# Optimization experiments

Hardware: AMD Instinct MI355X
Metric: run time of the kernel (lower is better)

## Reference

```python
import jax, jax.numpy as jnp
import numpy as np

EPS = 1e-6  # GLOBAL_EPS
D_QK = 192
ATTN_DIM = 768


def setup_inputs() -> dict:
    key = jax.random.key(0)
    ks = jax.random.split(key, 12)
    B, C, H, W = 16, 192, 56, 56
    d_qk, d_v = D_QK, 2 * D_QK
    attn_dim, inner = ATTN_DIM, d_v
    r = lambda k, s, sc=0.05: jax.random.normal(k, s, dtype=jnp.float32) * sc
    return {
        "x": jax.random.normal(ks[0], (B, C, H, W), dtype=jnp.float32),
        "proj_w": r(ks[1], (attn_dim, C)),          # 1x1 conv + BN folded
        "proj_b": r(ks[2], (attn_dim,)),
        "dwc_w": r(ks[3], (attn_dim, 1, 3, 3)),     # depthwise 3x3, BN folded
        "dwc_b": r(ks[4], (attn_dim,)),
        "g_w": r(ks[5], (inner, attn_dim)),          # ConvGate pointwise conv1d
        "g_b": r(ks[6], (inner,)),
        "an_w": 1.0 + r(ks[7], (inner,)),            # RMSNorm weight
        "sv": 1.0 + r(ks[8], (inner,)),              # Scale(inner, (1, inner, 1))
        "out_w": r(ks[9], (C, inner)),               # 1x1 conv + BN folded
        "out_b": r(ks[10], (C,)),
    }


def reference(x, proj_w, proj_b, dwc_w, dwc_b, g_w, g_b, an_w, sv, out_w, out_b):
    B, C, H, W = x.shape
    d_qk = D_QK
    # proj: ConvNorm 1x1 (conv + BN folded to affine)
    y = jnp.einsum("bchw,oc->bohw", x, proj_w) + proj_b[None, :, None, None]
    # dwc: RepConv depthwise 3x3 with residual (res=True)
    dw = jax.lax.conv_general_dilated(
        y, dwc_w, window_strides=(1, 1), padding="SAME",
        dimension_numbers=("NCHW", "OIHW", "NCHW"),
        feature_group_count=ATTN_DIM)
    y = dw + dwc_b[None, :, None, None] + y
    # flatten spatial -> tokens, split q/k/v along channels
    xs = y.reshape(B, ATTN_DIM, H * W)            # (B, attn_dim, N)
    q, k, v = xs[:, :d_qk], xs[:, d_qk:2 * d_qk], xs[:, 2 * d_qk:]
    # linear_attn: feature map = silu, scale = N**-0.5
    qf = jax.nn.silu(q)                            # (B, d_qk, N)
    kf = jax.nn.silu(k)
    N = H * W
    s = N ** -0.5
    # use_linear branch (N >> d): z = kT.mean(-2,True) @ q + eps ; attn = (v s)(kT s) q
    z = jnp.einsum("bd,bdn->bn", kf.mean(-1), qf)[:, None, :] + EPS  # (B, 1, N)
    vk = jnp.einsum("bvn,bdn->bvd", v * s, kf * s)  # (B, d_v, d_qk)
    attn = jnp.einsum("bvd,bdn->bvn", vk, qf) / z   # (B, d_v, N)
    # gate: pointwise conv1d on full projected features + sigmoid
    gate = jax.nn.sigmoid(jnp.einsum("bcn,oc->bon", xs, g_w) + g_b[None, :, None])
    attn = attn * gate
    # attn_norm (RMS over channels) + scale_v(v) residual
    rms = jnp.sqrt(jnp.mean(attn * attn, axis=1, keepdims=True) + EPS)
    attn = attn / rms * an_w[None, :, None] + v * sv[None, :, None]
    # out: ConvNorm 1x1 back to dim
    o = attn.reshape(B, -1, H, W)
    return jnp.einsum("bchw,oc->bohw", o, out_w) + out_b[None, :, None, None]
```

## Files before the change

kernel.cpp:

```cpp
#include <hip/hip_runtime.h>
#include <hip/hip_bf16.h>

typedef unsigned short u16;
typedef __attribute__((ext_vector_type(8))) short bf16x8;
typedef __attribute__((ext_vector_type(4))) float f32x4;

constexpr int B_ = 16, C_ = 192, H_ = 56, W_ = 56;
constexpr int N_ = H_ * W_;
constexpr int NP = 3200;
constexpr int A_ = 768;
constexpr int Dq = 192;
constexpr int Vd = 384;
constexpr float EPSf = 1e-6f;

union U8 { bf16x8 v; u16 s[8]; unsigned u[4]; };

__device__ __forceinline__ float bits2f(u16 u) {
  return __uint_as_float(((unsigned)u) << 16);
}
__device__ __forceinline__ u16 f2bits(float f) {
  __hip_bfloat16 h = __float2bfloat16(f);
  u16 u;
  __builtin_memcpy(&u, &h, sizeof(u));
  return u;
}
__device__ __forceinline__ float silu_f(float v) { return v / (1.0f + __expf(-v)); }
__device__ __forceinline__ float sigm_f(float v) { return 1.0f / (1.0f + __expf(-v)); }

__device__ __forceinline__ f32x4 MFMA(bf16x8 a, bf16x8 b, f32x4 c) {
  return __builtin_amdgcn_mfma_f32_16x16x32_bf16(a, b, c, 0, 0, 0);
}
__device__ __forceinline__ int swz(int row) { return (row & 7) ^ ((row >> 3) & 7); }

__global__ __launch_bounds__(256) void k_prep(const float* __restrict__ pw,
                                              const float* __restrict__ gw,
                                              const float* __restrict__ ow,
                                              u16* __restrict__ pwb,
                                              u16* __restrict__ gwb,
                                              u16* __restrict__ owb) {
  const int bid = blockIdx.x;
  const size_t base = ((size_t)bid * 256 + threadIdx.x) * 8;
  const float* src;
  u16* dst;
  size_t off;
  if (bid < 72) { src = pw; dst = pwb; off = base; }
  else if (bid < 216) { src = gw; dst = gwb; off = base - 147456; }
  else { src = ow; dst = owb; off = base - 442368; }
  float4 v0 = *(const float4*)&src[off];
  float4 v1 = *(const float4*)&src[off + 4];
  U8 r;
  r.s[0] = f2bits(v0.x); r.s[1] = f2bits(v0.y); r.s[2] = f2bits(v0.z); r.s[3] = f2bits(v0.w);
  r.s[4] = f2bits(v1.x); r.s[5] = f2bits(v1.y); r.s[6] = f2bits(v1.z); r.s[7] = f2bits(v1.w);
  *(bf16x8*)&dst[off] = r.v;
}

__global__ __launch_bounds__(256) void k_proj(const float* __restrict__ x,
                                              const u16* __restrict__ pwb,
                                              const float* __restrict__ pb,
                                              u16* __restrict__ y0t) {
  const int n0 = blockIdx.x * 64;
  const int oy = blockIdx.y;
  const int b = blockIdx.z;
  __shared__ u16 Xt[64][200];
  __shared__ u16 Wa[256][32];
  const int t = threadIdx.x;
  const int lane = t & 63, wid = t >> 6;
  const int fr = lane & 15, fg = lane >> 4;

  {
    const int p = t & 31, co = t >> 5;
    const float* xb = x + (size_t)b * C_ * N_ + n0 + 2 * p;
#pragma unroll
    for (int rnd = 0; rnd < 3; ++rnd) {
      const int c0 = rnd * 64 + co * 8;
      float2 v[8];
#pragma unroll
      for (int i = 0; i < 8; ++i) v[i] = *(const float2*)&xb[(size_t)(c0 + i) * N_];
      U8 r0, r1;
#pragma unroll
      for (int i = 0; i < 8; ++i) { r0.s[i] = f2bits(v[i].x); r1.s[i] = f2bits(v[i].y); }
      *(bf16x8*)&Xt[2 * p][c0] = r0.v;
      *(bf16x8*)&Xt[2 * p + 1][c0] = r1.v;
    }
  }

  f32x4 acc[4][4];
#pragma unroll
  for (int mi = 0; mi < 4; ++mi)
#pragma unroll
    for (int ni = 0; ni < 4; ++ni) acc[mi][ni] = (f32x4){0.f, 0.f, 0.f, 0.f};

  const int orow_c = t >> 2, oct_c = t & 3;
  U8 wreg[4];
#pragma unroll
  for (int jj = 0; jj < 4; ++jj)
    wreg[jj].v = *(const bf16x8*)&pwb[(size_t)(oy * 256 + orow_c + 64 * jj) * C_ + oct_c * 8];

  for (int ks = 0; ks < 6; ++ks) {
    __syncthreads();
#pragma unroll
    for (int jj = 0; jj < 4; ++jj) {
      const int orow = orow_c + 64 * jj;
      const int sw = (orow >> 1) & 3;
      *(bf16x8*)&Wa[orow][(oct_c ^ sw) * 8] = wreg[jj].v;
    }
    __syncthreads();
    if (ks < 5) {
#pragma unroll
      for (int jj = 0; jj < 4; ++jj)
        wreg[jj].v = *(const bf16x8*)&pwb[(size_t)(oy * 256 + orow_c + 64 * jj) * C_ +
                                          (ks + 1) * 32 + oct_c * 8];
    }
    bf16x8 bfrag[4];
#pragma unroll
    for (int ni = 0; ni < 4; ++ni)
      bfrag[ni] = *(const bf16x8*)&Xt[ni * 16 + fr][ks * 32 + fg * 8];
    __builtin_amdgcn_s_setprio(1);
#pragma unroll
    for (int mi = 0; mi < 4; ++mi) {
      const int ar = wid * 64 + mi * 16 + fr;
      bf16x8 a = *(const bf16x8*)&Wa[ar][(fg ^ ((ar >> 1) & 3)) * 8];
#pragma unroll
      for (int ni = 0; ni < 4; ++ni) acc[mi][ni] = MFMA(a, bfrag[ni], acc[mi][ni]);
    }
    __builtin_amdgcn_s_setprio(0);
  }
#pragma unroll
  for (int mi = 0; mi < 4; ++mi) {
    const int o4 = oy * 256 + wid * 64 + mi * 16 + fg * 4;
    const float b0 = pb[o4], b1 = pb[o4 + 1], b2 = pb[o4 + 2], b3 = pb[o4 + 3];
#pragma unroll
    for (int ni = 0; ni < 4; ++ni) {
      const int n = n0 + ni * 16 + fr;
      ushort4 pk;
      pk.x = f2bits(acc[mi][ni][0] + b0);
      pk.y = f2bits(acc[mi][ni][1] + b1);
      pk.z = f2bits(acc[mi][ni][2] + b2);
      pk.w = f2bits(acc[mi][ni][3] + b3);
      *(ushort4*)&y0t[((size_t)b * NP + n) * A_ + o4] = pk;
    }
  }
}

__global__ __launch_bounds__(256) void k_dwc(const u16* __restrict__ y0t,
                                             const float* __restrict__ cw,
                                             const float* __restrict__ cb,
                                             u16* __restrict__ yt) {
  const int pid = blockIdx.x;
  const int L = (pid & 7) * 336 + (pid >> 3);
  const int h = L % 56, at = (L / 56) % 3, b = L / 168;
  const int t = threadIdx.x;
  const int a = at * 256 + (t & 31) * 8;
  const int wl = t >> 5;
  float w9[9][8];
  float bias[8];
#pragma unroll
  for (int j = 0; j < 8; ++j) {
    bias[j] = cb[a + j];
#pragma unroll
    for (int k = 0; k < 9; ++k) w9[k][j] = cw[(a + j) * 9 + k];
  }
  const u16* src = y0t + (size_t)b * NP * A_ + a;
  u16* dst = yt + (size_t)b * NP * A_ + a;
  const bool hok0 = h > 0, hok2 = h < 55;
  for (int wc = 0; wc < 7; ++wc) {
    const int w = wc * 8 + wl;
    const bool wok0 = w > 0, wok2 = w < 55;
    U8 nb[9];
#pragma unroll
    for (int dh = -1; dh <= 1; ++dh) {
      const bool hok = (dh == -1) ? hok0 : ((dh == 1) ? hok2 : true);
#pragma unroll
      for (int dw = -1; dw <= 1; ++dw) {
        const int k = (dh + 1) * 3 + (dw + 1);
        const bool ok = hok && ((dw == -1) ? wok0 : ((dw == 1) ? wok2 : true));
        if (ok)
          nb[k].v = *(const bf16x8*)&src[(size_t)((h + dh) * 56 + (w + dw)) * A_];
        else
          nb[k].u[0] = nb[k].u[1] = nb[k].u[2] = nb[k].u[3] = 0u;
      }
    }
    U8 o;
#pragma unroll
    for (int j = 0; j < 8; ++j) {
      float s = bias[j] + bits2f(nb[4].s[j]);
#pragma unroll
      for (int k = 0; k < 9; ++k) s = fmaf(w9[k][j], bits2f(nb[k].s[j]), s);
      o.s[j] = f2bits(s);
    }
    *(bf16x8*)&dst[(size_t)(h * 56 + w) * A_] = o.v;
  }
}

__global__ __launch_bounds__(256) void k_kfmean(const u16* __restrict__ yt,
                                                float* __restrict__ kfp) {
  const int ns = blockIdx.x, dc = blockIdx.y, b = blockIdx.z;
  const int t = threadIdx.x;
  const int dq = t & 15, nw = t >> 4;
  const u16* p = yt + ((size_t)b * NP + ns * 448 + nw) * A_ + 192 + dc * 64 + dq * 4;
  float s0 = 0, s1 = 0, s2 = 0, s3 = 0;
#pragma unroll 4
  for (int i = 0; i < 28; ++i) {
    ushort4 u = *(const ushort4*)&p[(size_t)i * 16 * A_];
    s0 += silu_f(bits2f(u.x));
    s1 += silu_f(bits2f(u.y));
    s2 += silu_f(bits2f(u.z));
    s3 += silu_f(bits2f(u.w));
  }
  __shared__ float red[16][65];
  red[nw][dq * 4 + 0] = s0;
  red[nw][dq * 4 + 1] = s1;
  red[nw][dq * 4 + 2] = s2;
  red[nw][dq * 4 + 3] = s3;
  __syncthreads();
  if (t < 64) {
    float s = 0;
#pragma unroll
    for (int i = 0; i < 16; ++i) s += red[i][t];
    kfp[((size_t)ns * B_ + b) * Dq + dc * 64 + t] = s * (1.0f / (float)N_);
  }
}

__global__ __launch_bounds__(256) void k_z(const u16* __restrict__ yt,
                                           const float* __restrict__ kfp,
                                           float* __restrict__ zinv,
                                           float* __restrict__ ssq) {
  const int b = blockIdx.y;
  const int n = blockIdx.x * 256 + threadIdx.x;
  __shared__ float kf[192];
  if (threadIdx.x < 192) {
    float s = 0;
#pragma unroll
    for (int ns = 0; ns < 7; ++ns) s += kfp[((size_t)ns * B_ + b) * Dq + threadIdx.x];
    kf[threadIdx.x] = s;
  }
  __syncthreads();
  if (n < NP) {
    if (n < N_) {
      const u16* p = yt + ((size_t)b * NP + n) * A_;
      float z = 0;
#pragma unroll
      for (int j = 0; j < 24; ++j) {
        U8 u;
        u.v = *(const bf16x8*)&p[j * 8];
#pragma unroll
        for (int i = 0; i < 8; ++i) z = fmaf(kf[j * 8 + i], silu_f(bits2f(u.s[i])), z);
      }
      zinv[(size_t)b * NP + n] = 1.0f / (z + EPSf);
    } else {
      zinv[(size_t)b * NP + n] = 0.f;
    }
    ssq[(size_t)b * NP + n] = 0.f;
  }
}

__global__ __launch_bounds__(256) void k_vk(const u16* __restrict__ yt,
                                            float* __restrict__ vkpart) {
  const int pid = blockIdx.x;
  const int L = (pid & 7) * 42 + (pid >> 3);
  const int ns = L % 7;
  const int vblk = (L / 7) % 3;
  const int b = L / 21;
  const int t = threadIdx.x;
  const int lane = t & 63, wid = t >> 6;
  const int fr = lane & 15, fg = lane >> 4;
  const int vbase = (wid >> 1) * 64, dbase = (wid & 1) * 96;

  __shared__ u16 T[320 * 64];
  unsigned* T32 = (unsigned*)T;

  const int oct0 = t & 7;
  const int pair = (t >> 3) & 31;
  const int nb0 = ns * 448;

  U8 pre[5][2];
  auto load_pre = [&](int n0) {
    const int n = nb0 + n0 + pair * 2;
#pragma unroll
    for (int j = 0; j < 5; ++j) {
      const int oct = oct0 + 8 * j;
      const u16* srcp;
      if (j < 3)
        srcp = yt + ((size_t)b * NP + n) * A_ + 192 + oct * 8;
      else
        srcp = yt + ((size_t)b * NP + n) * A_ + 384 + vblk * 128 + (oct - 24) * 8;
      pre[j][0].v = *(const bf16x8*)srcp;
      pre[j][1].v = *(const bf16x8*)(srcp + A_);
      if (j < 3) {
#pragma unroll
        for (int i = 0; i < 8; ++i) {
          pre[j][0].s[i] = f2bits(silu_f(bits2f(pre[j][0].s[i])));
          pre[j][1].s[i] = f2bits(silu_f(bits2f(pre[j][1].s[i])));
        }
      }
    }
  };

  f32x4 acc[4][6];
#pragma unroll
  for (int mi = 0; mi < 4; ++mi)
#pragma unroll
    for (int ni = 0; ni < 6; ++ni) acc[mi][ni] = (f32x4){0.f, 0.f, 0.f, 0.f};

  load_pre(0);
  for (int s = 0; s < 7; ++s) {
    __syncthreads();
#pragma unroll
    for (int j = 0; j < 5; ++j) {
      const int rowb = (oct0 + 8 * j) * 8;
#pragma unroll
      for (int i = 0; i < 8; ++i) {
        const int row = rowb + i;
        const int sw = swz(row);
        const unsigned val =
            ((unsigned)pre[j][0].s[i] & 0xffffu) | (((unsigned)pre[j][1].s[i]) << 16);
        T32[row * 32 + (pair ^ (sw << 2))] = val;
      }
    }
    __syncthreads();
    if (s < 6) load_pre((s + 1) * 64);
    __builtin_amdgcn_s_setprio(1);
#pragma unroll
    for (int kf2 = 0; kf2 < 2; ++kf2) {
      bf16x8 bfrag[6];
#pragma unroll
      for (int ni = 0; ni < 6; ++ni) {
        const int row = dbase + ni * 16 + fr;
        bfrag[ni] = *(const bf16x8*)&T[row * 64 + ((kf2 * 32 + fg * 8) ^ (swz(row) << 3))];
      }
#pragma unroll
      for (int mi = 0; mi < 4; ++mi) {
        const int row = 192 + vbase + mi * 16 + fr;
        bf16x8 a = *(const bf16x8*)&T[row * 64 + ((kf2 * 32 + fg * 8) ^ (swz(row) << 3))];
#pragma unroll
        for (int ni = 0; ni < 6; ++ni) acc[mi][ni] = MFMA(a, bfrag[ni], acc[mi][ni]);
      }
    }
    __builtin_amdgcn_s_setprio(0);
  }
  float* base = vkpart + (((size_t)ns * 16 + b) * 3 + vblk) * (128 * 192);
#pragma unroll
  for (int mi = 0; mi < 4; ++mi)
#pragma unroll
    for (int ni = 0; ni < 6; ++ni) {
      const int v = vbase + mi * 16 + fg * 4;
      const int d = dbase + ni * 16 + fr;
      float* o = base + (size_t)v * 192 + d;
      o[0] = acc[mi][ni][0];
      o[192] = acc[mi][ni][1];
      o[384] = acc[mi][ni][2];
      o[576] = acc[mi][ni][3];
    }
}

__global__ __launch_bounds__(256) void k_vkred(const float* __restrict__ vkpart,
                                               u16* __restrict__ vkb) {
  const size_t e = ((size_t)blockIdx.x * 256 + threadIdx.x) * 8;
  constexpr size_t NSSTRIDE = (size_t)16 * 3 * 128 * 192;
  float4 s0 = {0, 0, 0, 0}, s1 = {0, 0, 0, 0};
#pragma unroll
  for (int ns = 0; ns < 7; ++ns) {
    float4 a0 = *(const float4*)&vkpart[ns * NSSTRIDE + e];
    float4 a1 = *(const float4*)&vkpart[ns * NSSTRIDE + e + 4];
    s0.x += a0.x; s0.y += a0.y; s0.z += a0.z; s0.w += a0.w;
    s1.x += a1.x; s1.y += a1.y; s1.z += a1.z; s1.w += a1.w;
  }
  const float sc = 1.0f / (float)N_;
  U8 r;
  r.s[0] = f2bits(s0.x * sc); r.s[1] = f2bits(s0.y * sc);
  r.s[2] = f2bits(s0.z * sc); r.s[3] = f2bits(s0.w * sc);
  r.s[4] = f2bits(s1.x * sc); r.s[5] = f2bits(s1.y * sc);
  r.s[6] = f2bits(s1.z * sc); r.s[7] = f2bits(s1.w * sc);
  *(bf16x8*)&vkb[e] = r.v;
}

__global__ __launch_bounds__(256, 2) void k_gateattn(const u16* __restrict__ yt,
                                                     const float* __restrict__ zinv,
                                                     const u16* __restrict__ vkb,
                                                     const u16* __restrict__ gwb,
                                                     const float* __restrict__ gb,
                                                     u16* __restrict__ attnt,
                                                     float* __restrict__ ssq) {
  const int pid = blockIdx.x;
  const int L = (pid & 7) * 100 + (pid >> 3);
  const int vh = L & 1;
  const int n0 = ((L >> 1) % 25) * 128;
  const int b = L / 50;
  const int t = threadIdx.x;
  const int lane = t & 63, wid = t >> 6, wm = wid >> 1, wn = wid & 1;
  const int fr = lane & 15, fg = lane >> 4;
  __shared__ u16 T[2][320 * 64];
  const u16* yb = yt + ((size_t)b * NP + n0) * A_;
  const u16* wb0 = vkb + ((size_t)b * Vd + vh * 192) * 192;
  const u16* wb1 = gwb + (size_t)(vh * 192) * A_;

  const int oct = t & 7, rowb = t >> 3;
  U8 pre[10];
  auto loadPre = [&](int nit) {
    if (nit < 3) {
      const int ks = nit * 64;
#pragma unroll
      for (int j = 0; j < 6; ++j)
        pre[j].v = *(const bf16x8*)&wb0[(size_t)(rowb + 32 * j) * 192 + ks + oct * 8];
#pragma unroll
      for (int j = 6; j < 10; ++j)
        pre[j].v = *(const bf16x8*)&yb[(size_t)(rowb + 32 * (j - 6)) * A_ + ks + oct * 8];
    } else {
      const int ks = (nit - 3) * 64;
#pragma unroll
      for (int j = 0; j < 6; ++j)
        pre[j].v = *(const bf16x8*)&wb1[(size_t)(rowb + 32 * j) * A_ + ks + oct * 8];
#pragma unroll
      for (int j = 6; j < 10; ++j)
        pre[j].v = *(const bf16x8*)&yb[(size_t)(rowb + 32 * (j - 6)) * A_ + ks + oct * 8];
    }
  };
  auto writeStage = [&](int nit, int buf) {
    const bool sl = (nit < 3);
    u16* Tb = &T[buf][0];
#pragma unroll
    for (int j = 0; j < 10; ++j) {
      const int r = rowb + 32 * j;
      U8 w = pre[j];
      if (sl && j >= 6) {
#pragma unroll
        for (int i = 0; i < 8; ++i) w.s[i] = f2bits(silu_f(bits2f(w.s[i])));
      }
      *(bf16x8*)&Tb[r * 64 + ((oct * 8) ^ (swz(r) << 3))] = w.v;
    }
  };

  f32x4 acc[6][4];
#pragma unroll
  for (int mi = 0; mi < 6; ++mi)
#pragma unroll
    for (int ni = 0; ni < 4; ++ni) acc[mi][ni] = (f32x4){0.f, 0.f, 0.f, 0.f};
  uint2 pp[6][4];

  loadPre(0);
  writeStage(0, 0);
  loadPre(1);
  __syncthreads();

  for (int it = 0; it < 15; ++it) {
    const int cur = it & 1;
    if (it < 14) writeStage(it + 1, cur ^ 1);
    if (it < 13) loadPre(it + 2);
    const u16* Tb = &T[cur][0];
    __builtin_amdgcn_s_setprio(1);
#pragma unroll
    for (int kf2 = 0; kf2 < 2; ++kf2) {
      bf16x8 bfr[4];
#pragma unroll
      for (int ni = 0; ni < 4; ++ni) {
        const int row = 192 + wn * 64 + ni * 16 + fr;
        bfr[ni] = *(const bf16x8*)&Tb[row * 64 + ((kf2 * 32 + fg * 8) ^ (swz(row) << 3))];
      }
#pragma unroll
      for (int mi = 0; mi < 6; ++mi) {
        const int row = wm * 96 + mi * 16 + fr;
        bf16x8 a = *(const bf16x8*)&Tb[row * 64 + ((kf2 * 32 + fg * 8) ^ (swz(row) << 3))];
#pragma unroll
        for (int ni = 0; ni < 4; ++ni) acc[mi][ni] = MFMA(a, bfr[ni], acc[mi][ni]);
      }
    }
    __builtin_amdgcn_s_setprio(0);
    if (it == 2) {
      float zv[4];
#pragma unroll
      for (int ni = 0; ni < 4; ++ni)
        zv[ni] = zinv[(size_t)b * NP + n0 + wn * 64 + ni * 16 + fr];
#pragma unroll
      for (int mi = 0; mi < 6; ++mi)
#pragma unroll
        for (int ni = 0; ni < 4; ++ni) {
          const float z = zv[ni];
          unsigned a0 = ((unsigned)f2bits(acc[mi][ni][0] * z) & 0xffffu) |
                        (((unsigned)f2bits(acc[mi][ni][1] * z) & 0xffffu) << 16);
          unsigned a1 = ((unsigned)f2bits(acc[mi][ni][2] * z) & 0xffffu) |
                        (((unsigned)f2bits(acc[mi][ni][3] * z) & 0xffffu) << 16);
          pp[mi][ni] = make_uint2(a0, a1);
          acc[mi][ni] = (f32x4){0.f, 0.f, 0.f, 0.f};
        }
    }
    __syncthreads();
  }

  float ssqa[4] = {0.f, 0.f, 0.f, 0.f};
#pragma unroll
  for (int mi = 0; mi < 6; ++mi) {
    const int vb = vh * 192 + wm * 96 + mi * 16 + fg * 4;
    const float g0 = gb[vb], g1 = gb[vb + 1], g2 = gb[vb + 2], g3 = gb[vb + 3];
#pragma unroll
    for (int ni = 0; ni < 4; ++ni) {
      const int n = n0 + wn * 64 + ni * 16 + fr;
      const uint2 p = pp[mi][ni];
      const float pv0 = bits2f((u16)(p.x & 0xffffu)), pv1 = bits2f((u16)(p.x >> 16));
      const float pv2 = bits2f((u16)(p.y & 0xffffu)), pv3 = bits2f((u16)(p.y >> 16));
      const float q0 = pv0 * sigm_f(acc[mi][ni][0] + g0);
      const float q1 = pv1 * sigm_f(acc[mi][ni][1] + g1);
      const float q2 = pv2 * sigm_f(acc[mi][ni][2] + g2);
      const float q3 = pv3 * sigm_f(acc[mi][ni][3] + g3);
      ushort4 o;
      o.x = f2bits(q0);
      o.y = f2bits(q1);
      o.z = f2bits(q2);
      o.w = f2bits(q3);
      *(ushort4*)&attnt[((size_t)b * NP + n) * Vd + vb] = o;
      ssqa[ni] += q0 * q0 + q1 * q1 + q2 * q2 + q3 * q3;
    }
  }
#pragma unroll
  for (int ni = 0; ni < 4; ++ni) {
    float ss = ssqa[ni];
    ss += __shfl_xor(ss, 16);
    ss += __shfl_xor(ss, 32);
    if (fg == 0) {
      const int n = n0 + wn * 64 + ni * 16 + fr;
      atomicAdd(&ssq[(size_t)b * NP + n], ss);
    }
  }
}

__global__ __launch_bounds__(256) void k_out(const u16* __restrict__ attnt,
                                             const u16* __restrict__ yt,
                                             const u16* __restrict__ owb,
                                             const float* __restrict__ ob,
                                             const float* __restrict__ anw,
                                             const float* __restrict__ svw,
                                             const float* __restrict__ ssq,
                                             float* __restrict__ out) {
  const int n0 = blockIdx.x * 64;
  const int b = blockIdx.y;
  __shared__ u16 T[256 * 64];
  __shared__ float anws[384], svws[384];
  __shared__ float rinv[64];
  const int t = threadIdx.x;
  const int lane = t & 63, wid = t >> 6, wm = wid >> 1, wn = wid & 1;
  const int fr = lane & 15, fg = lane >> 4;
  for (int i = t; i < 384; i += 256) {
    anws[i] = anw[i];
    svws[i] = svw[i];
  }
  if (t < 64)
    rinv[t] = rsqrtf(ssq[(size_t)b * NP + n0 + t] * (1.0f / (float)Vd) + EPSf);

  const int oct = t & 7, rowb = t >> 3;
  U8 preW[6], preA[2], preV[2];
  auto loadPre = [&](int it) {
    const int ks = it * 64;
#pragma unroll
    for (int j = 0; j < 6; ++j)
      preW[j].v = *(const bf16x8*)&owb[(size_t)(rowb + 32 * j) * Vd + ks + oct * 8];
#pragma unroll
    for (int j = 0; j < 2; ++j) {
      const int n = rowb + 32 * j;
      preA[j].v = *(const bf16x8*)&attnt[((size_t)b * NP + n0 + n) * Vd + ks + oct * 8];
      preV[j].v = *(const bf16x8*)&yt[((size_t)b * NP + n0 + n) * A_ + 384 + ks + oct * 8];
    }
  };

  f32x4 acc[6][2];
#pragma unroll
  for (int mi = 0; mi < 6; ++mi)
#pragma unroll
    for (int ni = 0; ni < 2; ++ni) acc[mi][ni] = (f32x4){0.f, 0.f, 0.f, 0.f};

  loadPre(0);
  __syncthreads();
  for (int it = 0; it < 6; ++it) {
#pragma unroll
    for (int j = 0; j < 6; ++j) {
      const int r = rowb + 32 * j;
      *(bf16x8*)&T[r * 64 + ((oct * 8) ^ (swz(r) << 3))] = preW[j].v;
    }
#pragma unroll
    for (int j = 0; j < 2; ++j) {
      const int n = rowb + 32 * j;
      const int r = 192 + n;
      const float ri = rinv[n];
      const int col0 = it * 64 + oct * 8;
      U8 o;
#pragma unroll
      for (int k = 0; k < 8; ++k)
        o.s[k] = f2bits(bits2f(preA[j].s[k]) * ri * anws[col0 + k] +
                        bits2f(preV[j].s[k]) * svws[col0 + k]);
      *(bf16x8*)&T[r * 64 + ((oct * 8) ^ (swz(r) << 3))] = o.v;
    }
    __syncthreads();
    if (it < 5) loadPre(it + 1);
    __builtin_amdgcn_s_setprio(1);
#pragma unroll
    for (int kf2 = 0; kf2 < 2; ++kf2) {
      bf16x8 bfr[2];
#pragma unroll
      for (int ni = 0; ni < 2; ++ni) {
        const int row = 192 + wn * 32 + ni * 16 + fr;
        bfr[ni] = *(const bf16x8*)&T[row * 64 + ((kf2 * 32 + fg * 8) ^ (swz(row) << 3))];
      }
#pragma unroll
      for (int mi = 0; mi < 6; ++mi) {
        const int row = wm * 96 + mi * 16 + fr;
        bf16x8 a = *(const bf16x8*)&T[row * 64 + ((kf2 * 32 + fg * 8) ^ (swz(row) << 3))];
        acc[mi][0] = MFMA(a, bfr[0], acc[mi][0]);
        acc[mi][1] = MFMA(a, bfr[1], acc[mi][1]);
      }
    }
    __builtin_amdgcn_s_setprio(0);
    if (it < 5) __syncthreads();
  }
#pragma unroll
  for (int mi = 0; mi < 6; ++mi) {
    const int c = wm * 96 + mi * 16 + fg * 4;
    const float b0 = ob[c], b1 = ob[c + 1], b2 = ob[c + 2], b3 = ob[c + 3];
#pragma unroll
    for (int ni = 0; ni < 2; ++ni) {
      const int n = n0 + wn * 32 + ni * 16 + fr;
      float* o = out + ((size_t)b * C_ + c) * N_ + n;
      o[0 * N_] = acc[mi][ni][0] + b0;
      o[1 * N_] = acc[mi][ni][1] + b1;
      o[2 * N_] = acc[mi][ni][2] + b2;
      o[3 * N_] = acc[mi][ni][3] + b3;
    }
  }
}

extern "C" void kernel_launch(void* const* d_in, const int* in_sizes, int n_in,
                              void* d_out, int out_size, void* d_ws, size_t ws_size,
                              hipStream_t stream) {
  (void)in_sizes; (void)n_in; (void)out_size; (void)ws_size;
  const float* x = (const float*)d_in[0];
  const float* pw = (const float*)d_in[1];
  const float* pb = (const float*)d_in[2];
  const float* cw = (const float*)d_in[3];
  const float* cb = (const float*)d_in[4];
  const float* gw = (const float*)d_in[5];
  const float* gb = (const float*)d_in[6];
  const float* anw = (const float*)d_in[7];
  const float* svw = (const float*)d_in[8];
  const float* ow = (const float*)d_in[9];
  const float* ob = (const float*)d_in[10];
  float* out = (float*)d_out;

  char* ws = (char*)d_ws;
  const size_t szY = (size_t)B_ * NP * A_ * 2;
  u16* y0t = (u16*)(ws);
  u16* attnt = (u16*)(ws);
  float* vkpart = (float*)(ws + 39321600);
  u16* vkb = (u16*)(ws + 72351744);
  u16* yt = (u16*)(ws + szY);
  char* ws2 = ws + 2 * szY;
  float* kfp = (float*)(ws2);
  float* zinv = (float*)(ws2 + 86016);
  float* ssq = (float*)(ws2 + 86016 + 204800);
  u16* pwb = (u16*)(ws2 + 86016 + 2 * 204800);
  u16* gwb = (u16*)(ws2 + 86016 + 2 * 204800 + 294912);
  u16* owb = (u16*)(ws2 + 86016 + 2 * 204800 + 294912 + 589824);

  k_prep<<<dim3(252), 256, 0, stream>>>(pw, gw, ow, pwb, gwb, owb);
  k_proj<<<dim3(49, 3, 16), 256, 0, stream>>>(x, pwb, pb, y0t);
  k_dwc<<<dim3(2688), 256, 0, stream>>>(y0t, cw, cb, yt);
  k_kfmean<<<dim3(7, 3, 16), 256, 0, stream>>>(yt, kfp);
  k_z<<<dim3(13, 16), 256, 0, stream>>>(yt, kfp, zinv, ssq);
  k_vk<<<dim3(336), 256, 0, stream>>>(yt, vkpart);
  k_vkred<<<dim3(576), 256, 0, stream>>>(vkpart, vkb);
  k_gateattn<<<dim3(800), 256, 0, stream>>>(yt, zinv, vkb, gwb, gb, attnt, ssq);
  k_out<<<dim3(49, 16), 256, 0, stream>>>(attnt, yt, owb, ob, anw, svw, ssq, out);
}
```

Baseline: 296.4 us.

## Fuse k-feature mean into depthwise conv and reuse sliding column loads

The depthwise conv kernel now walks seven consecutive w positions per thread with a sliding 3-column register window, so each input vector is loaded about once instead of nine times. It also accumulates silu of the k channels and reduces them into a per-batch kfp buffer with atomics. This removes the separate k-feature-mean kernel and its re-read of yt. The padded NP stride is replaced by N_ for y0t/yt, which requires clamped row indices in the gate/attn loads. The kfp buffer is zeroed by an extra block in the prep kernel, and k_gateattn loses its min-blocks-per-CU launch bound.

```diff
diff --git a/kernel.cpp b/kernel.cpp
--- a/kernel.cpp
+++ b/kernel.cpp
@@ -37,8 +37,13 @@
                                               const float* __restrict__ ow,
                                               u16* __restrict__ pwb,
                                               u16* __restrict__ gwb,
-                                              u16* __restrict__ owb) {
+                                              u16* __restrict__ owb,
+                                              float* __restrict__ kfp) {
   const int bid = blockIdx.x;
+  if (bid == 252) {
+    for (int i = threadIdx.x; i < B_ * Dq; i += 256) kfp[i] = 0.f;
+    return;
+  }
   const size_t base = ((size_t)bid * 256 + threadIdx.x) * 8;
   const float* src;
   u16* dst;
@@ -137,7 +142,7 @@
       pk.y = f2bits(acc[mi][ni][1] + b1);
       pk.z = f2bits(acc[mi][ni][2] + b2);
       pk.w = f2bits(acc[mi][ni][3] + b3);
-      *(ushort4*)&y0t[((size_t)b * NP + n) * A_ + o4] = pk;
+      *(ushort4*)&y0t[((size_t)b * N_ + n) * A_ + o4] = pk;
     }
   }
 }
@@ -145,13 +150,14 @@
 __global__ __launch_bounds__(256) void k_dwc(const u16* __restrict__ y0t,
                                              const float* __restrict__ cw,
                                              const float* __restrict__ cb,
-                                             u16* __restrict__ yt) {
+                                             u16* __restrict__ yt,
+                                             float* __restrict__ kfp) {
   const int pid = blockIdx.x;
   const int L = (pid & 7) * 336 + (pid >> 3);
   const int h = L % 56, at = (L / 56) % 3, b = L / 168;
   const int t = threadIdx.x;
   const int a = at * 256 + (t & 31) * 8;
-  const int wl = t >> 5;
+  const int ws0 = (t >> 5) * 7;
   float w9[9][8];
   float bias[8];
 #pragma unroll
@@ -160,64 +166,64 @@
 #pragma unroll
     for (int k = 0; k < 9; ++k) w9[k][j] = cw[(a + j) * 9 + k];
   }
-  const u16* src = y0t + (size_t)b * NP * A_ + a;
-  u16* dst = yt + (size_t)b * NP * A_ + a;
+  const u16* src = y0t + (size_t)b * N_ * A_ + a;
+  u16* dst = yt + (size_t)b * N_ * A_ + a;
   const bool hok0 = h > 0, hok2 = h < 55;
-  for (int wc = 0; wc < 7; ++wc) {
-    const int w = wc * 8 + wl;
-    const bool wok0 = w > 0, wok2 = w < 55;
-    U8 nb[9];
-#pragma unroll
-    for (int dh = -1; dh <= 1; ++dh) {
-      const bool hok = (dh == -1) ? hok0 : ((dh == 1) ? hok2 : true);
-#pragma unroll
-      for (int dw = -1; dw <= 1; ++dw) {
-        const int k = (dh + 1) * 3 + (dw + 1);
-        const bool ok = hok && ((dw == -1) ? wok0 : ((dw == 1) ? wok2 : true));
-        if (ok)
-          nb[k].v = *(const bf16x8*)&src[(size_t)((h + dh) * 56 + (w + dw)) * A_];
-        else
-          nb[k].u[0] = nb[k].u[1] = nb[k].u[2] = nb[k].u[3] = 0u;
-      }
-    }
+
+  U8 cm[3], cc[3], cp[3];
+  auto zero8 = [](U8& x) { x.u[0] = x.u[1] = x.u[2] = x.u[3] = 0u; };
+  auto loadcol = [&](U8 col[3], int w) {
+    if ((unsigned)w < 56u) {
+      if (hok0) col[0].v = *(const bf16x8*)&src[(size_t)((h - 1) * 56 + w) * A_];
+      else zero8(col[0]);
+      col[1].v = *(const bf16x8*)&src[(size_t)(h * 56 + w) * A_];
+      if (hok2) col[2].v = *(const bf16x8*)&src[(size_t)((h + 1) * 56 + w) * A_];
+      else zero8(col[2]);
+    } else {
+      zero8(col[0]); zero8(col[1]); zero8(col[2]);
+    }
+  };
+  loadcol(cm, ws0 - 1);
+  loadcol(cc, ws0);
+
+  float kacc[8] = {0.f, 0.f, 0.f, 0.f, 0.f, 0.f, 0.f, 0.f};
+#pragma unroll
+  for (int i = 0; i < 7; ++i) {
+    const int w = ws0 + i;
+    loadcol(cp, w + 1);
     U8 o;
 #pragma unroll
     for (int j = 0; j < 8; ++j) {
-      float s = bias[j] + bits2f(nb[4].s[j]);
-#pragma unroll
-      for (int k = 0; k < 9; ++k) s = fmaf(w9[k][j], bits2f(nb[k].s[j]), s);
+      float s = bias[j] + bits2f(cc[1].s[j]);
+      s = fmaf(w9[0][j], bits2f(cm[0].s[j]), s);
+      s = fmaf(w9[1][j], bits2f(cc[0].s[j]), s);
+      s = fmaf(w9[2][j], bits2f(cp[0].s[j]), s);
+      s = fmaf(w9[3][j], bits2f(cm[1].s[j]), s);
+      s = fmaf(w9[4][j], bits2f(cc[1].s[j]), s);
+      s = fmaf(w9[5][j], bits2f(cp[1].s[j]), s);
+      s = fmaf(w9[6][j], bits2f(cm[2].s[j]), s);
+      s = fmaf(w9[7][j], bits2f(cc[2].s[j]), s);
+      s = fmaf(w9[8][j], bits2f(cp[2].s[j]), s);
       o.s[j] = f2bits(s);
+      const int ch = a + j;
+      if (ch >= 192 && ch < 384) kacc[j] += silu_f(s);
     }
     *(bf16x8*)&dst[(size_t)(h * 56 + w) * A_] = o.v;
-  }
-}
-
-__global__ __launch_bounds__(256) void k_kfmean(const u16* __restrict__ yt,
-                                                float* __restrict__ kfp) {
-  const int ns = blockIdx.x, dc = blockIdx.y, b = blockIdx.z;
-  const int t = threadIdx.x;
-  const int dq = t & 15, nw = t >> 4;
-  const u16* p = yt + ((size_t)b * NP + ns * 448 + nw) * A_ + 192 + dc * 64 + dq * 4;
-  float s0 = 0, s1 = 0, s2 = 0, s3 = 0;
-#pragma unroll 4
-  for (int i = 0; i < 28; ++i) {
-    ushort4 u = *(const ushort4*)&p[(size_t)i * 16 * A_];
-    s0 += silu_f(bits2f(u.x));
-    s1 += silu_f(bits2f(u.y));
-    s2 += silu_f(bits2f(u.z));
-    s3 += silu_f(bits2f(u.w));
-  }
-  __shared__ float red[16][65];
-  red[nw][dq * 4 + 0] = s0;
-  red[nw][dq * 4 + 1] = s1;
-  red[nw][dq * 4 + 2] = s2;
-  red[nw][dq * 4 + 3] = s3;
-  __syncthreads();
-  if (t < 64) {
-    float s = 0;
-#pragma unroll
-    for (int i = 0; i < 16; ++i) s += red[i][t];
-    kfp[((size_t)ns * B_ + b) * Dq + dc * 64 + t] = s * (1.0f / (float)N_);
+#pragma unroll
+    for (int r = 0; r < 3; ++r) { cm[r] = cc[r]; cc[r] = cp[r]; }
+  }
+
+  __shared__ float red[8][256];
+  if (at < 2) {
+    const int cbase = (t & 31) * 8, wl = t >> 5;
+#pragma unroll
+    for (int j = 0; j < 8; ++j) red[wl][cbase + j] = kacc[j];
+    __syncthreads();
+    float s = 0.f;
+#pragma unroll
+    for (int i = 0; i < 8; ++i) s += red[i][t];
+    const int ac = at * 256 + t;
+    if (ac >= 192 && ac < 384) atomicAdd(&kfp[b * Dq + (ac - 192)], s);
   }
 }
 
@@ -228,16 +234,12 @@
   const int b = blockIdx.y;
   const int n = blockIdx.x * 256 + threadIdx.x;
   __shared__ float kf[192];
-  if (threadIdx.x < 192) {
-    float s = 0;
-#pragma unroll
-    for (int ns = 0; ns < 7; ++ns) s += kfp[((size_t)ns * B_ + b) * Dq + threadIdx.x];
-    kf[threadIdx.x] = s;
-  }
+  if (threadIdx.x < 192)
+    kf[threadIdx.x] = kfp[b * Dq + threadIdx.x] * (1.0f / (float)N_);
   __syncthreads();
   if (n < NP) {
     if (n < N_) {
-      const u16* p = yt + ((size_t)b * NP + n) * A_;
+      const u16* p = yt + ((size_t)b * N_ + n) * A_;
       float z = 0;
 #pragma unroll
       for (int j = 0; j < 24; ++j) {
@@ -281,9 +283,9 @@
       const int oct = oct0 + 8 * j;
       const u16* srcp;
       if (j < 3)
-        srcp = yt + ((size_t)b * NP + n) * A_ + 192 + oct * 8;
+        srcp = yt + ((size_t)b * N_ + n) * A_ + 192 + oct * 8;
       else
-        srcp = yt + ((size_t)b * NP + n) * A_ + 384 + vblk * 128 + (oct - 24) * 8;
+        srcp = yt + ((size_t)b * N_ + n) * A_ + 384 + vblk * 128 + (oct - 24) * 8;
       pre[j][0].v = *(const bf16x8*)srcp;
       pre[j][1].v = *(const bf16x8*)(srcp + A_);
       if (j < 3) {
@@ -374,13 +376,13 @@
   *(bf16x8*)&vkb[e] = r.v;
 }
 
-__global__ __launch_bounds__(256, 2) void k_gateattn(const u16* __restrict__ yt,
-                                                     const float* __restrict__ zinv,
-                                                     const u16* __restrict__ vkb,
-                                                     const u16* __restrict__ gwb,
-                                                     const float* __restrict__ gb,
-                                                     u16* __restrict__ attnt,
-                                                     float* __restrict__ ssq) {
+__global__ __launch_bounds__(256) void k_gateattn(const u16* __restrict__ yt,
+                                                  const float* __restrict__ zinv,
+                                                  const u16* __restrict__ vkb,
+                                                  const u16* __restrict__ gwb,
+                                                  const float* __restrict__ gb,
+                                                  u16* __restrict__ attnt,
+                                                  float* __restrict__ ssq) {
   const int pid = blockIdx.x;
   const int L = (pid & 7) * 100 + (pid >> 3);
   const int vh = L & 1;
@@ -390,7 +392,7 @@
   const int lane = t & 63, wid = t >> 6, wm = wid >> 1, wn = wid & 1;
   const int fr = lane & 15, fg = lane >> 4;
   __shared__ u16 T[2][320 * 64];
-  const u16* yb = yt + ((size_t)b * NP + n0) * A_;
+  const u16* yb = yt + (size_t)b * N_ * A_;
   const u16* wb0 = vkb + ((size_t)b * Vd + vh * 192) * 192;
   const u16* wb1 = gwb + (size_t)(vh * 192) * A_;
 
@@ -403,16 +405,20 @@
       for (int j = 0; j < 6; ++j)
         pre[j].v = *(const bf16x8*)&wb0[(size_t)(rowb + 32 * j) * 192 + ks + oct * 8];
 #pragma unroll
-      for (int j = 6; j < 10; ++j)
-        pre[j].v = *(const bf16x8*)&yb[(size_t)(rowb + 32 * (j - 6)) * A_ + ks + oct * 8];
+      for (int j = 6; j < 10; ++j) {
+        const int n = min(n0 + rowb + 32 * (j - 6), N_ - 1);
+        pre[j].v = *(const bf16x8*)&yb[(size_t)n * A_ + ks + oct * 8];
+      }
     } else {
       const int ks = (nit - 3) * 64;
 #pragma unroll
       for (int j = 0; j < 6; ++j)
         pre[j].v = *(const bf16x8*)&wb1[(size_t)(rowb + 32 * j) * A_ + ks + oct * 8];
 #pragma unroll
-      for (int j = 6; j < 10; ++j)
-        pre[j].v = *(const bf16x8*)&yb[(size_t)(rowb + 32 * (j - 6)) * A_ + ks + oct * 8];
+      for (int j = 6; j < 10; ++j) {
+        const int n = min(n0 + rowb + 32 * (j - 6), N_ - 1);
+        pre[j].v = *(const bf16x8*)&yb[(size_t)n * A_ + ks + oct * 8];
+      }
     }
   };
   auto writeStage = [&](int nit, int buf) {
@@ -556,7 +562,7 @@
     for (int j = 0; j < 2; ++j) {
       const int n = rowb + 32 * j;
       preA[j].v = *(const bf16x8*)&attnt[((size_t)b * NP + n0 + n) * Vd + ks + oct * 8];
-      preV[j].v = *(const bf16x8*)&yt[((size_t)b * NP + n0 + n) * A_ + 384 + ks + oct * 8];
+      preV[j].v = *(const bf16x8*)&yt[((size_t)b * N_ + n0 + n) * A_ + 384 + ks + oct * 8];
     }
   };
 
@@ -643,7 +649,7 @@
   float* out = (float*)d_out;
 
   char* ws = (char*)d_ws;
-  const size_t szY = (size_t)B_ * NP * A_ * 2;
+  const size_t szY = (size_t)B_ * N_ * A_ * 2;
   u16* y0t = (u16*)(ws);
   u16* attnt = (u16*)(ws);
   float* vkpart = (float*)(ws + 39321600);
@@ -657,10 +663,9 @@
   u16* gwb = (u16*)(ws2 + 86016 + 2 * 204800 + 294912);
   u16* owb = (u16*)(ws2 + 86016 + 2 * 204800 + 294912 + 589824);
 
-  k_prep<<<dim3(252), 256, 0, stream>>>(pw, gw, ow, pwb, gwb, owb);
+  k_prep<<<dim3(253), 256, 0, stream>>>(pw, gw, ow, pwb, gwb, owb, kfp);
   k_proj<<<dim3(49, 3, 16), 256, 0, stream>>>(x, pwb, pb, y0t);
-  k_dwc<<<dim3(2688), 256, 0, stream>>>(y0t, cw, cb, yt);
-  k_kfmean<<<dim3(7, 3, 16), 256, 0, stream>>>(yt, kfp);
+  k_dwc<<<dim3(2688), 256, 0, stream>>>(y0t, cw, cb, yt, kfp);
   k_z<<<dim3(13, 16), 256, 0, stream>>>(yt, kfp, zinv, ssq);
   k_vk<<<dim3(336), 256, 0, stream>>>(yt, vkpart);
   k_vkred<<<dim3(576), 256, 0, stream>>>(vkpart, vkb);
```

After: 323.7 us. 9.2% more time.
